# Kernel tuning notes

Measured on AMD Instinct MI355X. Metric: run time of the kernel, lower is better.

## Reference

```python
import jax, jax.numpy as jnp
import numpy as np

S = 4        # patch stride
G = 4        # offset groups
C = 1024     # token channels = 64*4*4
CG = C // G  # 256 channels per group


def _conv2d(x, w, b, pad, groups=1):
    y = jax.lax.conv_general_dilated(x, w, (1, 1), [(pad, pad), (pad, pad)],
                                     dimension_numbers=('NCHW', 'OIHW', 'NCHW'),
                                     feature_group_count=groups)
    return y if b is None else y + b.reshape(1, -1, 1, 1)


def _ln_c(x, g, b, eps=1e-5):
    # LayerNormProxy: LayerNorm over the channel dim of NCHW
    mu = jnp.mean(x, axis=1, keepdims=True)
    var = jnp.mean((x - mu) ** 2, axis=1, keepdims=True)
    return (x - mu) * jax.lax.rsqrt(var + eps) * g.reshape(1, -1, 1, 1) + b.reshape(1, -1, 1, 1)


def _l2norm(x, axis, eps=1e-12):
    n = jnp.sqrt(jnp.sum(x * x, axis=axis, keepdims=True))
    return x / jnp.maximum(n, eps)


def _gs_nearest(img, grid):
    # F.grid_sample(mode='nearest', padding_mode='zeros', align_corners=True)
    B, Cc, H, W = img.shape
    x = (grid[..., 0] + 1.0) * 0.5 * (W - 1)
    y = (grid[..., 1] + 1.0) * 0.5 * (H - 1)
    xi = jnp.round(x).astype(jnp.int32)
    yi = jnp.round(y).astype(jnp.int32)
    valid = ((xi >= 0) & (xi < W) & (yi >= 0) & (yi < H)).astype(img.dtype)
    xc = jnp.clip(xi, 0, W - 1)
    yc = jnp.clip(yi, 0, H - 1)
    vals = jax.vmap(lambda im, yy, xx: im[:, yy, xx])(img, yc, xc)  # (B,C,Hg,Wg)
    return vals * valid[:, None]


def _gs_bilinear(img, grid):
    # F.grid_sample(mode='bilinear', padding_mode='zeros', align_corners=True)
    B, Cc, H, W = img.shape
    x = (grid[..., 0] + 1.0) * 0.5 * (W - 1)
    y = (grid[..., 1] + 1.0) * 0.5 * (H - 1)
    x0 = jnp.floor(x)
    y0 = jnp.floor(y)
    wx1 = x - x0
    wy1 = y - y0

    def tap(yf, xf, wgt):
        xi = xf.astype(jnp.int32)
        yi = yf.astype(jnp.int32)
        valid = ((xf >= 0) & (xf < W) & (yf >= 0) & (yf < H)).astype(img.dtype)
        xc = jnp.clip(xi, 0, W - 1)
        yc = jnp.clip(yi, 0, H - 1)
        v = jax.vmap(lambda im, yy, xx: im[:, yy, xx])(img, yc, xc)
        return v * (valid * wgt)[:, None]

    return (tap(y0, x0, (1 - wy1) * (1 - wx1)) + tap(y0, x0 + 1, (1 - wy1) * wx1)
            + tap(y0 + 1, x0, wy1 * (1 - wx1)) + tap(y0 + 1, x0 + 1, wy1 * wx1))


def _unfold_s(x):
    # F.unfold(kernel=(S,S), stride=S): (n,c,h,w) -> (n, c*S*S, (h/S)*(w/S))
    n, c, h, w = x.shape
    x = x.reshape(n, c, h // S, S, w // S, S).transpose(0, 1, 3, 5, 2, 4)
    return x.reshape(n, c * S * S, (h // S) * (w // S))


def _fold_s(x, h, w):
    # F.fold, inverse of _unfold_s (no overlap since kernel == stride)
    n, cl, L = x.shape
    c = cl // (S * S)
    x = x.reshape(n, c, S, S, h // S, w // S).transpose(0, 1, 4, 2, 5, 3)
    return x.reshape(n, c, h, w)


def _ref_points(Hk, Wk, dtype):
    ry = (jnp.linspace(0.5, Hk - 0.5, Hk, dtype=dtype) / Hk) * 2.0 - 1.0
    rx = (jnp.linspace(0.5, Wk - 0.5, Wk, dtype=dtype) / Wk) * 2.0 - 1.0
    gy, gx = jnp.meshgrid(ry, rx, indexing='ij')
    return jnp.stack([gy, gx], -1)  # (Hk, Wk, 2) ordered (y, x)


def _forward(curr_feat, index_feat_set_s1, anchor_feat, s1, s2, s3, location_feat,
             fusion_w, fusion_b, to_dw_w, to_dw_b, to_ln_w, to_ln_b, to_pw_w):
    n, c, h, w = curr_feat.shape
    t = s1.shape[1]
    H4, W4 = h // S, w // S
    feat_len = c * S * S          # 1024
    feat_num = H4 * W4

    # build normalized flow grid (x, y) from location map
    gf = location_feat.reshape(n, t, 2, H4, W4).transpose(0, 1, 3, 4, 2)
    gx = 2.0 * gf[..., 0] / max(W4 - 1, 1) - 1.0
    gy = 2.0 * gf[..., 1] / max(H4 - 1, 1) - 1.0
    grid = jnp.stack([gx, gy], -1).reshape(n * t, H4, W4, 2)

    o1 = _gs_nearest(s1.reshape(n * t, feat_len, H4, W4), grid)
    o2 = _gs_nearest(s2.reshape(n * t, feat_len, H4, W4), grid)
    o3 = _gs_nearest(s3.reshape(n * t, feat_len, H4, W4), grid)
    idx = _gs_nearest(index_feat_set_s1.reshape(n * t, feat_len, H4, W4), grid)

    # index tokens -> (n, feat_num, t, C), L2-normalized over C
    idx = idx.reshape(n, t, feat_len, feat_num).transpose(0, 3, 1, 2)
    idx = _l2norm(idx, 3)

    # current-frame tokens -> (n, feat_num, C), L2-normalized
    cf = _unfold_s(curr_feat).transpose(0, 2, 1)
    cf = _l2norm(cf, 2)

    temporal_q = cf.reshape(n, H4, W4, C).transpose(0, 3, 1, 2)                       # (n, C, H4, W4)
    temporal_k = idx.transpose(0, 2, 1, 3).reshape(n * t, H4, W4, C).transpose(0, 3, 1, 2)

    # offset subnetwork (time_offset)
    q_off = jnp.tile(temporal_q.reshape(n * G, CG, H4, W4), (t, 1, 1, 1))            # repeat(t,1,1,1)
    k_off = temporal_k.reshape(n * t * G, CG, H4, W4)
    off = jnp.concatenate([q_off, k_off], axis=1)                                     # (n*t*G, 2*CG, H4, W4)
    o = _conv2d(off, to_dw_w, to_dw_b, 2, groups=CG)
    o = jax.nn.gelu(_ln_c(o, to_ln_w, to_ln_b), approximate=False)
    offset = _conv2d(o, to_pw_w, None, 0)                                             # (n*t*G, 2, Hk, Wk)
    Hk, Wk = offset.shape[2], offset.shape[3]
    orange = jnp.array([1.0 / Hk, 1.0 / Wk], dtype=offset.dtype).reshape(1, 2, 1, 1)
    offset = jnp.tanh(offset) * orange * 2.0                                          # offset_range_factor = 2
    pos = offset.transpose(0, 2, 3, 1) + _ref_points(Hk, Wk, offset.dtype)[None]      # (y, x)
    grid2 = pos[..., ::-1]                                                            # (x, y)

    # deformable sampling of temporal keys, cosine QK attention (max over t)
    tks = _gs_bilinear(temporal_k.reshape(n * t * G, CG, Hk, Wk), grid2)
    tks = tks.reshape(n, t, G, CG, Hk, Wk).transpose(0, 4, 5, 1, 2, 3).reshape(n, Hk * Wk, t, C)
    matrix_index = jnp.einsum('nltc,nlc->nlt', tks, cf)                               # (n, feat_num, t)
    corr_soft = jnp.max(matrix_index, axis=2)
    corr_index = jnp.argmax(matrix_index, axis=2)
    corr_soft_map = _fold_s(jnp.broadcast_to(corr_soft[:, None, :], (n, feat_len, feat_num)), h, w)

    def sample_gather(ox):
        v = _gs_bilinear(ox.reshape(n * t * G, CG, H4, W4), grid2)
        v = v.reshape(n, t, feat_len, feat_num)
        v = jnp.take_along_axis(v, corr_index[:, None, None, :], axis=1)[:, 0]
        return _fold_s(v, h, w)

    f1 = sample_gather(o1)
    f2 = sample_gather(o2)
    f3 = sample_gather(o3)

    out = _conv2d(jnp.concatenate([f1, f2, f3], axis=1), fusion_w, fusion_b, 1)
    out = out * corr_soft_map + anchor_feat
    return out


def setup_inputs() -> dict:
    key = jax.random.key(0)
    ks = jax.random.split(key, 12)
    n, t, h, w, c = 2, 12, 96, 96, 64
    H4, W4 = h // 4, w // 4
    fl = c * 16
    f = lambda k, sh, s=1.0: jax.random.normal(k, sh, dtype=jnp.float32) * s
    return {
        'curr_feat': f(ks[0], (n, c, h, w)),
        'index_feat_set_s1': f(ks[1], (n, t, fl, H4, W4)),
        'anchor_feat': f(ks[2], (n, c, h, w)),
        'sparse_feat_set_s1': f(ks[3], (n, t, fl, H4, W4)),
        'sparse_feat_set_s2': f(ks[4], (n, t, fl, H4, W4)),
        'sparse_feat_set_s3': f(ks[5], (n, t, fl, H4, W4)),
        'location_feat': jax.random.uniform(ks[6], (n, 2 * t, H4, W4), dtype=jnp.float32) * W4,
        'fusion_w': f(ks[7], (64, 192, 3, 3), 0.02),
        'fusion_b': jnp.zeros((64,), jnp.float32),
        'to_dw_w': f(ks[8], (256, 2, 5, 5), 0.05),
        'to_dw_b': jnp.zeros((256,), jnp.float32),
        'to_ln_w': jnp.ones((256,), jnp.float32),
        'to_ln_b': jnp.zeros((256,), jnp.float32),
        'to_pw_w': f(ks[9], (2, 256, 1, 1), 0.05),
    }


def reference(curr_feat, index_feat_set_s1, anchor_feat, sparse_feat_set_s1,
              sparse_feat_set_s2, sparse_feat_set_s3, location_feat,
              fusion_w, fusion_b, to_dw_w, to_dw_b, to_ln_w, to_ln_b, to_pw_w):
    return _forward(curr_feat, index_feat_set_s1, anchor_feat, sparse_feat_set_s1,
                    sparse_feat_set_s2, sparse_feat_set_s3, location_feat,
                    fusion_w, fusion_b, to_dw_w, to_dw_b, to_ln_w, to_ln_b, to_pw_w)
```

## Files before the change

kernel.cpp:

```cpp
#include <hip/hip_runtime.h>
#include <hip/hip_bf16.h>
#include <math.h>

#define NN 2
#define TT 12
#define HH 96
#define WW 96
#define CC 64
#define H4 24
#define W4 24
#define FL 1024
#define FN 576

typedef short short8 __attribute__((ext_vector_type(8)));
typedef float f32x4 __attribute__((ext_vector_type(4)));

__device__ __forceinline__ float u2f(unsigned short u){
  unsigned int x = ((unsigned int)u)<<16; float f; __builtin_memcpy(&f,&x,4); return f;
}
__device__ __forceinline__ unsigned short f2u(float f){
  __hip_bfloat16 b = __float2bfloat16(f); unsigned short u; __builtin_memcpy(&u,&b,2); return u;
}

__global__ void k_map(const float* __restrict__ loc, int* __restrict__ smap){
  int i = blockIdx.x*256 + threadIdx.x;
  if (i >= NN*TT*FN) return;
  int nt = i / FN, pix = i % FN;
  int ni = nt / TT, ti = nt % TT;
  const float* lp = loc + ((size_t)ni*(2*TT) + 2*ti)*FN + pix;
  float vx = lp[0];
  float vy = lp[FN];
  float gx = (2.0f*vx)/23.0f - 1.0f;
  float gy = (2.0f*vy)/23.0f - 1.0f;
  float x = ((gx + 1.0f)*0.5f)*23.0f;
  float y = ((gy + 1.0f)*0.5f)*23.0f;
  int xi = (int)rintf(x);
  int yi = (int)rintf(y);
  bool valid = (xi>=0)&&(xi<W4)&&(yi>=0)&&(yi<H4);
  smap[i] = valid ? (yi*W4+xi) : -1;
}

__global__ void k_part(const float* __restrict__ idxf, float* __restrict__ part){
  int blk = blockIdx.x;
  int nt = blk >> 4, ch0 = (blk & 15)*64;
  int pix = threadIdx.x;
  const float* p = idxf + ((size_t)nt*FL + ch0)*FN + pix;
  float s = 0.f;
  for (int c=0;c<64;c++){ float v = p[(size_t)c*FN]; s += v*v; }
  part[(size_t)blk*FN + pix] = s;
}
__global__ void k_norm(const float* __restrict__ part, float* __restrict__ nrm){
  int i = blockIdx.x*256+threadIdx.x;
  if (i>=NN*TT*FN) return;
  int nt = i/FN, pix = i%FN;
  float s=0.f;
  for (int c=0;c<16;c++) s += part[(size_t)(nt*16+c)*FN + pix];
  nrm[i] = sqrtf(s);
}

__global__ void k_cf(const float* __restrict__ curr, float* __restrict__ cf){
  int blk = blockIdx.x;
  int ni = blk/FN, l = blk%FN;
  int by = l/W4, bx = l%W4;
  int tid = threadIdx.x;
  int ci = tid>>2, sy = tid&3;
  const float* p = curr + (((size_t)ni*CC+ci)*HH + by*4+sy)*WW + bx*4;
  float4 v = *(const float4*)p;
  float s = v.x*v.x+v.y*v.y+v.z*v.z+v.w*v.w;
  __shared__ float red[256];
  red[tid]=s; __syncthreads();
  for(int o=128;o>0;o>>=1){ if(tid<o) red[tid]+=red[tid+o]; __syncthreads(); }
  float r = 1.0f/fmaxf(sqrtf(red[0]),1e-12f);
  float4 o4 = make_float4(v.x*r, v.y*r, v.z*r, v.w*r);
  ((float4*)(cf + (size_t)blk*FL))[tid] = o4;
}

__global__ __launch_bounds__(256) void k_tr_idx(const float* __restrict__ idxf,
    const float* __restrict__ nrm, float* __restrict__ idxT){
  int b = blockIdx.x;
  int cht = b & 15; int b2 = b >> 4;
  int pixt = b2 % 9; int nt = b2 / 9;
  int tid = threadIdx.x;
  __shared__ float t[64][65];
  #pragma unroll
  for (int r=0; r<16; ++r){
    int ch_l = r*4 + (tid>>6), pix_l = tid & 63;
    t[ch_l][pix_l] = idxf[((size_t)nt*FL + cht*64 + ch_l)*FN + pixt*64 + pix_l];
  }
  __syncthreads();
  #pragma unroll
  for (int r=0; r<16; ++r){
    int pix_l = r*4 + (tid>>6), ch_l = tid & 63;
    int gpix = pixt*64 + pix_l;
    float inv = 1.0f/fmaxf(nrm[nt*FN + gpix], 1e-12f);
    idxT[((size_t)nt*FN + gpix)*FL + cht*64 + ch_l] = t[ch_l][pix_l]*inv;
  }
}

__global__ __launch_bounds__(256) void k_tr_s(const float* __restrict__ s1,
    const float* __restrict__ s2, const float* __restrict__ s3,
    unsigned short* __restrict__ sT){
  int b = blockIdx.x;
  int tens = b / 3456; int bb = b % 3456;
  int cht = bb & 15; int b2 = bb >> 4;
  int pixt = b2 % 9; int nt = b2 / 9;
  const float* src = (tens==0)? s1 : (tens==1)? s2 : s3;
  int tid = threadIdx.x;
  __shared__ float t[64][65];
  #pragma unroll
  for (int r=0; r<16; ++r){
    int ch_l = r*4 + (tid>>6), pix_l = tid & 63;
    t[ch_l][pix_l] = src[((size_t)nt*FL + cht*64 + ch_l)*FN + pixt*64 + pix_l];
  }
  __syncthreads();
  #pragma unroll
  for (int r=0; r<16; ++r){
    int pix_l = r*4 + (tid>>6), ch_l = tid & 63;
    int gpix = pixt*64 + pix_l;
    sT[((size_t)(tens*NN*TT + nt)*FN + gpix)*FL + cht*64 + ch_l] = f2u(t[ch_l][pix_l]);
  }
}

__global__ void k_wpack(const float* __restrict__ fw, unsigned short* __restrict__ wp){
  int idx = blockIdx.x*256 + threadIdx.x;
  if (idx >= 9*6*4*64*8) return;
  int j = idx & 7; int t2 = idx >> 3;
  int L = t2 & 63; int t3 = t2 >> 6;
  int ntl = t3 & 3; int t4 = t3 >> 2;
  int kc = t4 % 6; int tap = t4 / 6;
  int dy = tap/3, dx = tap%3;
  int n = ntl*16 + (L & 15);
  int quad = L >> 4;
  int k = kc*32 + quad*8 + j;
  wp[idx] = f2u(fw[((size_t)n*192 + k)*9 + dy*3 + dx]);
}

__global__ __launch_bounds__(256) void k_offnet(
    const float* __restrict__ cf, const float* __restrict__ idxT,
    const int* __restrict__ smap,
    const float* __restrict__ dw_w, const float* __restrict__ dw_b,
    const float* __restrict__ ln_w, const float* __restrict__ ln_b,
    const float* __restrict__ pw_w, float* __restrict__ grid2){
  int blk = blockIdx.x;
  int b = blk/H4, y = blk%H4;
  int i = threadIdx.x;
  float wA[25], wB[25];
  const float* wp = dw_w + (size_t)i*50;
  #pragma unroll
  for(int k=0;k<25;k++){ wA[k]=wp[k]; wB[k]=wp[25+k]; }
  const float* src; int choff; const int* smrow;
  if (i < 128){
    int n2 = (b>>2)&1, g2 = b&3;
    src = cf + (size_t)n2*FN*FL;
    choff = g2*256 + 2*i;
    smrow = nullptr;
  } else {
    int nk = b/48, tik = (b>>2)%12, gk = b&3;
    int nt = nk*TT + tik;
    src = idxT + (size_t)nt*FN*FL;
    choff = gk*256 + 2*(i-128);
    smrow = smap + nt*FN;
  }
  float acc[24];
  #pragma unroll
  for(int x=0;x<24;x++) acc[x]=0.f;
  for(int dy=0; dy<5; ++dy){
    int row = y + dy - 2;
    if (row >= 0 && row < H4){
      #pragma unroll
      for(int xx=0; xx<24; ++xx){
        int pixsrc = smrow ? smrow[row*W4+xx] : (row*W4+xx);
        float2 v = make_float2(0.f,0.f);
        if (pixsrc >= 0) v = *(const float2*)(src + (size_t)pixsrc*FL + choff);
        #pragma unroll
        for(int dd=0; dd<5; ++dd){
          int x = xx + 2 - dd;
          if (x>=0 && x<24)
            acc[x] += v.x*wA[dy*5+dd] + v.y*wB[dy*5+dd];
        }
      }
    }
  }
  float bias = dw_b[i];
  #pragma unroll
  for(int x=0;x<24;x++) acc[x]+=bias;
  __shared__ float lds[256*25];
  __shared__ float smean[24], srstd[24];
  #pragma unroll
  for(int x=0;x<24;x++) lds[i*25+x]=acc[x];
  __syncthreads();
  if (i<24){
    float s=0.f,s2=0.f;
    for(int j=0;j<256;j++){ float v=lds[j*25+i]; s+=v; s2+=v*v; }
    float mean = s*(1.0f/256.0f);
    float var = s2*(1.0f/256.0f) - mean*mean;
    smean[i]=mean; srstd[i]=rsqrtf(var+1e-5f);
  }
  __syncthreads();
  float gi = ln_w[i], bi = ln_b[i];
  #pragma unroll
  for(int x=0;x<24;x++){
    float v = (acc[x]-smean[x])*srstd[x]*gi + bi;
    float ge = 0.5f*v*(1.0f + erff(v*0.70710678118654752f));
    lds[i*25+x] = ge;
  }
  __syncthreads();
  if (i<24){
    float d0=0.f,d1=0.f;
    for(int j=0;j<256;j++){ float v=lds[j*25+i]; d0 += v*pw_w[j]; d1 += v*pw_w[256+j]; }
    float off0 = tanhf(d0)*(2.0f/24.0f);
    float off1 = tanhf(d1)*(2.0f/24.0f);
    float ry = (((float)y + 0.5f)/24.0f)*2.0f - 1.0f;
    float rx = (((float)i + 0.5f)/24.0f)*2.0f - 1.0f;
    float posy = off0 + ry, posx = off1 + rx;
    float px = ((posx + 1.0f)*0.5f)*23.0f;
    float py = ((posy + 1.0f)*0.5f)*23.0f;
    *(float2*)(grid2 + ((size_t)b*FN + y*W4 + i)*2) = make_float2(px, py);
  }
}

__global__ __launch_bounds__(256) void k_corr(const float* __restrict__ cf,
    const float* __restrict__ idxT, const int* __restrict__ smap,
    const float* __restrict__ grid2,
    float* __restrict__ cors, int* __restrict__ cori){
  int blk = blockIdx.x; int ni = blk/FN, l = blk%FN;
  int tid = threadIdx.x;
  int g = tid>>6;
  float4 cfv = ((const float4*)(cf + (size_t)blk*FL))[tid];
  __shared__ float red[4];
  float best=-3.4e38f; int bidx=0;
  for(int ti=0; ti<TT; ++ti){
    int nt = ni*TT+ti;
    float2 gr = *(const float2*)(grid2 + ((size_t)(ni*48 + ti*4 + g)*FN + l)*2);
    float x0f = floorf(gr.x), y0f = floorf(gr.y);
    float wx = gr.x - x0f, wy = gr.y - y0f;
    float partial = 0.f;
    #pragma unroll
    for(int tap=0; tap<4; ++tap){
      float xf = x0f + (float)(tap&1);
      float yf = y0f + (float)(tap>>1);
      float w = ((tap&1)? wx : 1.f-wx) * ((tap>>1)? wy : 1.f-wy);
      if (xf>=0.f && xf<24.f && yf>=0.f && yf<24.f){
        int xi=(int)xf, yi=(int)yf;
        int sp2 = smap[nt*FN + yi*W4+xi];
        if (sp2 >= 0){
          float4 tv = ((const float4*)(idxT + (size_t)(nt*FN + sp2)*FL))[tid];
          partial += w*(tv.x*cfv.x + tv.y*cfv.y + tv.z*cfv.z + tv.w*cfv.w);
        }
      }
    }
    for(int o=32;o>0;o>>=1) partial += __shfl_down(partial, o, 64);
    if ((tid&63)==0) red[tid>>6]=partial;
    __syncthreads();
    if (tid==0){
      float s = red[0]+red[1]+red[2]+red[3];
      if (s > best){ best=s; bidx=ti; }
    }
    __syncthreads();
  }
  if (tid==0){ cors[blk]=best; cori[blk]=bidx; }
}

__global__ __launch_bounds__(256) void k_gather(const float* __restrict__ s1,
    const float* __restrict__ s2, const float* __restrict__ s3,
    const unsigned short* __restrict__ sT, int use_t,
    const int* __restrict__ smap, const float* __restrict__ grid2,
    const int* __restrict__ cori, unsigned short* __restrict__ fcat){
  int blk = blockIdx.x; int ni = blk/FN, l = blk%FN;
  int tid = threadIdx.x;
  int g = tid>>6;
  int ts = cori[blk];
  int nt = ni*TT + ts;
  float2 gr = *(const float2*)(grid2 + ((size_t)(ni*48 + ts*4 + g)*FN + l)*2);
  float x0f = floorf(gr.x), y0f = floorf(gr.y);
  float wx = gr.x - x0f, wy = gr.y - y0f;
  int sp[4]; float wt[4];
  #pragma unroll
  for(int tap=0; tap<4; ++tap){
    float xf = x0f + (float)(tap&1), yf = y0f + (float)(tap>>1);
    float w = ((tap&1)? wx : 1.f-wx)*((tap>>1)? wy : 1.f-wy);
    bool v = (xf>=0.f && xf<24.f && yf>=0.f && yf<24.f);
    int xi=(int)xf, yi=(int)yf;
    int pp = v ? smap[nt*FN + yi*W4+xi] : -1;
    sp[tap] = (pp>=0)? pp : 0; wt[tap] = (v && pp>=0)? w : 0.f;
  }
  float a[3][4];
  #pragma unroll
  for(int t2=0;t2<3;t2++){ a[t2][0]=0.f;a[t2][1]=0.f;a[t2][2]=0.f;a[t2][3]=0.f; }
  if (use_t){
    #pragma unroll
    for(int tap=0;tap<4;++tap){
      float w = wt[tap];
      if (w != 0.f){
        #pragma unroll
        for(int t2=0;t2<3;t2++){
          const unsigned short* p = sT + ((size_t)(t2*NN*TT + nt)*FN + sp[tap])*FL + tid*4;
          ushort4 r = *(const ushort4*)p;
          a[t2][0] += w*u2f(r.x); a[t2][1] += w*u2f(r.y);
          a[t2][2] += w*u2f(r.z); a[t2][3] += w*u2f(r.w);
        }
      }
    }
  } else {
    size_t chbase = ((size_t)nt*FL + tid*4)*FN;
    const float* sa[3] = { s1+chbase, s2+chbase, s3+chbase };
    #pragma unroll
    for(int t2=0;t2<3;t2++){
      #pragma unroll
      for(int tap=0;tap<4;++tap){
        float w = wt[tap];
        if (w != 0.f){
          const float* p = sa[t2] + sp[tap];
          a[t2][0] += w*p[0]; a[t2][1] += w*p[FN];
          a[t2][2] += w*p[2*FN]; a[t2][3] += w*p[3*FN];
        }
      }
    }
  }
  __shared__ float ldsv[3*16*65];
  #pragma unroll
  for(int t2=0;t2<3;t2++){
    #pragma unroll
    for(int k=0;k<4;k++){
      int cl = tid*4 + k;
      ldsv[t2*1040 + (cl&15)*65 + (cl>>4)] = a[t2][k];
    }
  }
  __syncthreads();
  int by = l/W4, bx = l%W4;
  int subpix = tid>>4, j = tid&15;
  int sy = subpix>>2, sx = subpix&3;
  unsigned short tmp[12];
  #pragma unroll
  for(int kk=0;kk<12;kk++){
    int ch = j*12+kk; int t2 = ch>>6; int ci = ch&63;
    tmp[kk] = f2u(ldsv[t2*1040 + subpix*65 + ci]);
  }
  unsigned short* dst = fcat + (((size_t)(ni*HH + by*4+sy))*WW + bx*4+sx)*192 + j*12;
  uint2* d2 = (uint2*)dst;
  d2[0] = make_uint2((unsigned)tmp[0] | ((unsigned)tmp[1]<<16), (unsigned)tmp[2] | ((unsigned)tmp[3]<<16));
  d2[1] = make_uint2((unsigned)tmp[4] | ((unsigned)tmp[5]<<16), (unsigned)tmp[6] | ((unsigned)tmp[7]<<16));
  d2[2] = make_uint2((unsigned)tmp[8] | ((unsigned)tmp[9]<<16), (unsigned)tmp[10]| ((unsigned)tmp[11]<<16));
}

__global__ __launch_bounds__(256) void k_fusion_mfma(
    const unsigned short* __restrict__ fcat, const unsigned short* __restrict__ wpk,
    const float* __restrict__ fb, const float* __restrict__ cors,
    const float* __restrict__ anchor, float* __restrict__ out){
  int b = blockIdx.x;
  int ni = b/288; int rem = b%288; int y = rem/3, xb = rem%3; int x0 = xb*32;
  int tid = threadIdx.x;
  __shared__ __align__(16) char sbuf[40960];
  unsigned short* aT = (unsigned short*)sbuf;
  for (int i = tid; i < 3*34*48; i += 256){
    int ch4 = i % 48; int t2 = i / 48;
    int xx = t2 % 34; int rr = t2 / 34;
    int row = y - 1 + rr, sx = x0 - 1 + xx;
    uint2 v = make_uint2(0u, 0u);
    if (row >= 0 && row < HH && sx >= 0 && sx < WW)
      v = *(const uint2*)(fcat + (((size_t)(ni*HH + row))*WW + sx)*192 + ch4*4);
    *(uint2*)(aT + ((size_t)rr*34 + xx)*200 + ch4*4) = v;
  }
  __syncthreads();
  int wv = tid>>6, lane = tid&63;
  int mt = wv&1, np = wv>>1;
  int m = lane&15, quad = lane>>4;
  f32x4 c0 = {0.f,0.f,0.f,0.f}, c1 = {0.f,0.f,0.f,0.f};
  for (int tap=0; tap<9; ++tap){
    int dy = tap/3, dx = tap%3;
    const unsigned short* arow = aT + ((size_t)dy*34 + mt*16 + m + dx)*200 + quad*8;
    #pragma unroll
    for (int kc=0; kc<6; ++kc){
      short8 af = *(const short8*)(arow + kc*32);
      const unsigned short* bp = wpk + (size_t)((tap*6+kc)*4 + np*2)*512 + lane*8;
      short8 b0 = *(const short8*)(bp);
      short8 b1 = *(const short8*)(bp + 512);
      c0 = __builtin_amdgcn_mfma_f32_16x16x32_bf16(af, b0, c0, 0, 0, 0);
      c1 = __builtin_amdgcn_mfma_f32_16x16x32_bf16(af, b1, c1, 0, 0, 0);
    }
  }
  __syncthreads();
  float* oT = (float*)sbuf;
  #pragma unroll
  for (int r=0; r<4; ++r){
    int xl = mt*16 + quad*4 + r;
    oT[xl*65 + np*32 + m]      = c0[r];
    oT[xl*65 + np*32 + 16 + m] = c1[r];
  }
  __syncthreads();
  for (int i = tid; i < 2048; i += 256){
    int co = i >> 5, xl = i & 31;
    int x = x0 + xl;
    float csm = cors[ni*FN + (y>>2)*W4 + (x>>2)];
    size_t oidx = ((size_t)(ni*CC + co)*HH + y)*WW + x;
    out[oidx] = (oT[xl*65 + co] + fb[co])*csm + anchor[oidx];
  }
}

extern "C" void kernel_launch(void* const* d_in, const int* in_sizes, int n_in,
                              void* d_out, int out_size, void* d_ws, size_t ws_size,
                              hipStream_t stream) {
  const float* curr   = (const float*)d_in[0];
  const float* idxf   = (const float*)d_in[1];
  const float* anchor = (const float*)d_in[2];
  const float* s1 = (const float*)d_in[3];
  const float* s2 = (const float*)d_in[4];
  const float* s3 = (const float*)d_in[5];
  const float* loc = (const float*)d_in[6];
  const float* fw  = (const float*)d_in[7];
  const float* fb  = (const float*)d_in[8];
  const float* dww = (const float*)d_in[9];
  const float* dwb = (const float*)d_in[10];
  const float* lnw = (const float*)d_in[11];
  const float* lnb = (const float*)d_in[12];
  const float* pww = (const float*)d_in[13];
  char* ws = (char*)d_ws;
  const size_t MB = 1024*1024;
  int*            smap  = (int*)           (ws + 0);
  float*          nrm   = (float*)         (ws + 1*MB);
  float*          part  = (float*)         (ws + 2*MB);
  float*          cf    = (float*)         (ws + 3*MB);
  float*          idxT  = (float*)         (ws + 8*MB);
  float*          grid2 = (float*)         (ws + 62*MB);
  float*          cors  = (float*)         (ws + 63*MB);
  int*            cori  = (int*)           (ws + 63*MB + 8192);
  unsigned short* fcat  = (unsigned short*)(ws + 64*MB);
  unsigned short* wpk   = (unsigned short*)(ws + 71*MB);
  unsigned short* sT    = (unsigned short*)(ws + 72*MB);
  int use_t = (ws_size >= (size_t)(72*MB) + 84934656u) ? 1 : 0;
  float* out = (float*)d_out;

  k_map   <<<54,    256, 0, stream>>>(loc, smap);
  k_part  <<<384,   576, 0, stream>>>(idxf, part);
  k_norm  <<<54,    256, 0, stream>>>(part, nrm);
  k_cf    <<<1152,  256, 0, stream>>>(curr, cf);
  k_tr_idx<<<3456,  256, 0, stream>>>(idxf, nrm, idxT);
  if (use_t)
    k_tr_s<<<10368, 256, 0, stream>>>(s1, s2, s3, sT);
  k_wpack <<<432,   256, 0, stream>>>(fw, wpk);
  k_offnet<<<2304,  256, 0, stream>>>(cf, idxT, smap, dww, dwb, lnw, lnb, pww, grid2);
  k_corr  <<<1152,  256, 0, stream>>>(cf, idxT, smap, grid2, cors, cori);
  k_gather<<<1152,  256, 0, stream>>>(s1, s2, s3, sT, use_t, smap, grid2, cori, fcat);
  k_fusion_mfma<<<576, 256, 0, stream>>>(fcat, wpk, fb, cors, anchor, out);
}
```

Before: 541.2 us.

## Compute two output rows per offnet block and remap blocks for XCD locality

k_offnet now computes two adjacent output rows per block, so the six input rows loaded serve both rows instead of five rows per single output. This halves the block count and cuts redundant global loads of the depthwise-conv input. Both k_offnet and k_corr remap blockIdx so that blocks landing on the same XCD (index mod 8) work on the same batch or the same spatial band, aiming for better L2 reuse. The cost is doubled accumulator registers and an extra barrier per row, which may lower occupancy.

```diff
diff --git a/kernel.cpp b/kernel.cpp
--- a/kernel.cpp
+++ b/kernel.cpp
@@ -141,8 +141,10 @@
     const float* __restrict__ dw_w, const float* __restrict__ dw_b,
     const float* __restrict__ ln_w, const float* __restrict__ ln_b,
     const float* __restrict__ pw_w, float* __restrict__ grid2){
-  int blk = blockIdx.x;
-  int b = blk/H4, y = blk%H4;
+  int i0 = blockIdx.x;
+  int xcd = i0 & 7; int kk = i0 >> 3;
+  int b = (kk/12)*8 + xcd;
+  int y0 = 2*(kk%12);
   int i = threadIdx.x;
   float wA[25], wB[25];
   const float* wp = dw_w + (size_t)i*50;
@@ -161,61 +163,69 @@
     choff = gk*256 + 2*(i-128);
     smrow = smap + nt*FN;
   }
-  float acc[24];
-  #pragma unroll
-  for(int x=0;x<24;x++) acc[x]=0.f;
-  for(int dy=0; dy<5; ++dy){
-    int row = y + dy - 2;
-    if (row >= 0 && row < H4){
+  float acc[2][24];
+  #pragma unroll
+  for(int x=0;x<24;x++){ acc[0][x]=0.f; acc[1][x]=0.f; }
+  for(int r = y0-2; r <= y0+3; ++r){
+    if (r < 0 || r >= H4) continue;
+    int dy0 = r - y0 + 2;
+    int dy1 = dy0 - 1;
+    bool u0 = (dy0 < 5), u1 = (dy1 >= 0);
+    #pragma unroll
+    for(int xx=0; xx<24; ++xx){
+      int pixsrc = smrow ? smrow[r*W4+xx] : (r*W4+xx);
+      float2 v = make_float2(0.f,0.f);
+      if (pixsrc >= 0) v = *(const float2*)(src + (size_t)pixsrc*FL + choff);
       #pragma unroll
-      for(int xx=0; xx<24; ++xx){
-        int pixsrc = smrow ? smrow[row*W4+xx] : (row*W4+xx);
-        float2 v = make_float2(0.f,0.f);
-        if (pixsrc >= 0) v = *(const float2*)(src + (size_t)pixsrc*FL + choff);
-        #pragma unroll
-        for(int dd=0; dd<5; ++dd){
-          int x = xx + 2 - dd;
-          if (x>=0 && x<24)
-            acc[x] += v.x*wA[dy*5+dd] + v.y*wB[dy*5+dd];
+      for(int dd=0; dd<5; ++dd){
+        int x = xx + 2 - dd;
+        if (x>=0 && x<24){
+          if (u0) acc[0][x] += v.x*wA[dy0*5+dd] + v.y*wB[dy0*5+dd];
+          if (u1) acc[1][x] += v.x*wA[dy1*5+dd] + v.y*wB[dy1*5+dd];
         }
       }
     }
   }
   float bias = dw_b[i];
   #pragma unroll
-  for(int x=0;x<24;x++) acc[x]+=bias;
+  for(int x=0;x<24;x++){ acc[0][x]+=bias; acc[1][x]+=bias; }
   __shared__ float lds[256*25];
   __shared__ float smean[24], srstd[24];
-  #pragma unroll
-  for(int x=0;x<24;x++) lds[i*25+x]=acc[x];
-  __syncthreads();
-  if (i<24){
-    float s=0.f,s2=0.f;
-    for(int j=0;j<256;j++){ float v=lds[j*25+i]; s+=v; s2+=v*v; }
-    float mean = s*(1.0f/256.0f);
-    float var = s2*(1.0f/256.0f) - mean*mean;
-    smean[i]=mean; srstd[i]=rsqrtf(var+1e-5f);
-  }
-  __syncthreads();
   float gi = ln_w[i], bi = ln_b[i];
   #pragma unroll
-  for(int x=0;x<24;x++){
-    float v = (acc[x]-smean[x])*srstd[x]*gi + bi;
-    float ge = 0.5f*v*(1.0f + erff(v*0.70710678118654752f));
-    lds[i*25+x] = ge;
-  }
-  __syncthreads();
-  if (i<24){
-    float d0=0.f,d1=0.f;
-    for(int j=0;j<256;j++){ float v=lds[j*25+i]; d0 += v*pw_w[j]; d1 += v*pw_w[256+j]; }
-    float off0 = tanhf(d0)*(2.0f/24.0f);
-    float off1 = tanhf(d1)*(2.0f/24.0f);
-    float ry = (((float)y + 0.5f)/24.0f)*2.0f - 1.0f;
-    float rx = (((float)i + 0.5f)/24.0f)*2.0f - 1.0f;
-    float posy = off0 + ry, posx = off1 + rx;
-    float px = ((posx + 1.0f)*0.5f)*23.0f;
-    float py = ((posy + 1.0f)*0.5f)*23.0f;
-    *(float2*)(grid2 + ((size_t)b*FN + y*W4 + i)*2) = make_float2(px, py);
+  for(int yy=0; yy<2; ++yy){
+    int y = y0 + yy;
+    #pragma unroll
+    for(int x=0;x<24;x++) lds[i*25+x]=acc[yy][x];
+    __syncthreads();
+    if (i<24){
+      float s=0.f,s2=0.f;
+      for(int j=0;j<256;j++){ float v=lds[j*25+i]; s+=v; s2+=v*v; }
+      float mean = s*(1.0f/256.0f);
+      float var = s2*(1.0f/256.0f) - mean*mean;
+      smean[i]=mean; srstd[i]=rsqrtf(var+1e-5f);
+    }
+    __syncthreads();
+    #pragma unroll
+    for(int x=0;x<24;x++){
+      float v = (acc[yy][x]-smean[x])*srstd[x]*gi + bi;
+      float ge = 0.5f*v*(1.0f + erff(v*0.70710678118654752f));
+      lds[i*25+x] = ge;
+    }
+    __syncthreads();
+    if (i<24){
+      float d0=0.f,d1=0.f;
+      for(int j=0;j<256;j++){ float v=lds[j*25+i]; d0 += v*pw_w[j]; d1 += v*pw_w[256+j]; }
+      float off0 = tanhf(d0)*(2.0f/24.0f);
+      float off1 = tanhf(d1)*(2.0f/24.0f);
+      float ry = (((float)y + 0.5f)/24.0f)*2.0f - 1.0f;
+      float rx = (((float)i + 0.5f)/24.0f)*2.0f - 1.0f;
+      float posy = off0 + ry, posx = off1 + rx;
+      float px = ((posx + 1.0f)*0.5f)*23.0f;
+      float py = ((posy + 1.0f)*0.5f)*23.0f;
+      *(float2*)(grid2 + ((size_t)b*FN + y*W4 + i)*2) = make_float2(px, py);
+    }
+    __syncthreads();
   }
 }
 
@@ -223,7 +233,12 @@
     const float* __restrict__ idxT, const int* __restrict__ smap,
     const float* __restrict__ grid2,
     float* __restrict__ cors, int* __restrict__ cori){
-  int blk = blockIdx.x; int ni = blk/FN, l = blk%FN;
+  int i0 = blockIdx.x;
+  int band = i0 & 7; int k0 = i0 >> 3;
+  int ni = k0/72; int r0 = k0%72;
+  int y = band*3 + r0/24; int xx = r0%24;
+  int l = y*24 + xx;
+  int blk = ni*FN + l;
   int tid = threadIdx.x;
   int g = tid>>6;
   float4 cfv = ((const float4*)(cf + (size_t)blk*FL))[tid];
@@ -438,7 +453,7 @@
   if (use_t)
     k_tr_s<<<10368, 256, 0, stream>>>(s1, s2, s3, sT);
   k_wpack <<<432,   256, 0, stream>>>(fw, wpk);
-  k_offnet<<<2304,  256, 0, stream>>>(cf, idxT, smap, dww, dwb, lnw, lnb, pww, grid2);
+  k_offnet<<<1152,  256, 0, stream>>>(cf, idxT, smap, dww, dwb, lnw, lnb, pww, grid2);
   k_corr  <<<1152,  256, 0, stream>>>(cf, idxT, smap, grid2, cors, cori);
   k_gather<<<1152,  256, 0, stream>>>(s1, s2, s3, sT, use_t, smap, grid2, cori, fcat);
   k_fusion_mfma<<<576, 256, 0, stream>>>(fcat, wpk, fb, cors, anchor, out);
```

Measured after the change: 558.2 us. 1.03x slower.
